# Performance work log

Measured on AMD Instinct MI355X. Metric: run time of the kernel, lower is better.

The kernel has to match this reference:

```python
import jax, jax.numpy as jnp
import numpy as np

B, L, D, H, DFF, MAXD = 4, 2048, 1024, 16, 4096, 512
HD = D // H


def layer_norm(x, gamma, beta, eps=1e-5):
    mu = jnp.mean(x, axis=-1, keepdims=True)
    var = jnp.mean(jnp.square(x - mu), axis=-1, keepdims=True)
    return (x - mu) * jax.lax.rsqrt(var + eps) * gamma + beta


def setup_inputs() -> dict:
    key = jax.random.key(0)
    ks = jax.random.split(key, 8)
    s = 0.02
    return {
        "x": jax.random.normal(ks[0], (B, L, D), jnp.float32),
        "w_qkv": jax.random.normal(ks[1], (D, 3 * D), jnp.float32) * s,
        "w_out": jax.random.normal(ks[2], (D, D), jnp.float32) * s,
        "b_out": jnp.zeros((D,), jnp.float32),
        "bias_table": jax.random.normal(ks[3], (2 * MAXD - 1, H), jnp.float32) * s,
        "gamma1": jnp.ones((D,), jnp.float32),
        "beta1": jnp.zeros((D,), jnp.float32),
        "w_ff1": jax.random.normal(ks[4], (D, DFF), jnp.float32) * s,
        "b_ff1": jnp.zeros((DFF,), jnp.float32),
        "w_ff2": jax.random.normal(ks[5], (DFF, D), jnp.float32) * s,
        "b_ff2": jnp.zeros((D,), jnp.float32),
        "gamma2": jnp.ones((D,), jnp.float32),
        "beta2": jnp.zeros((D,), jnp.float32),
    }


def reference(x, w_qkv, w_out, b_out, bias_table, gamma1, beta1,
              w_ff1, b_ff1, w_ff2, b_ff2, gamma2, beta2):
    b, l, c = x.shape
    scale = HD ** -0.5
    qkv = x @ w_qkv  # [B,L,3D]
    q, k, v = jnp.split(qkv, 3, axis=-1)
    # [B,H,L,hd]
    q = q.reshape(b, l, H, HD).transpose(0, 2, 1, 3)
    k = k.reshape(b, l, H, HD).transpose(0, 2, 1, 3)
    v = v.reshape(b, l, H, HD).transpose(0, 2, 1, 3)
    scores = jnp.einsum("bhqd,bhkd->bhqk", q, k) * scale
    # relative position bias: [H,L,L]
    coords = jnp.arange(l)
    rel = jnp.clip(coords[None, :] - coords[:, None] + MAXD - 1, 0, 2 * MAXD - 2)
    bias = bias_table[rel].transpose(2, 0, 1)
    scores = scores + bias[None]
    attn = jax.nn.softmax(scores, axis=-1)
    ctx = jnp.einsum("bhqk,bhkd->bhqd", attn, v)
    ctx = ctx.transpose(0, 2, 1, 3).reshape(b, l, c)
    attn_out = ctx @ w_out + b_out
    x = layer_norm(x + attn_out, gamma1, beta1)
    h = jax.nn.gelu(x @ w_ff1 + b_ff1, approximate=False)
    ffn_out = h @ w_ff2 + b_ff2
    x = layer_norm(x + ffn_out, gamma2, beta2)
    return x
```

## Files before the change

kernel.cpp:

```cpp
#include <hip/hip_runtime.h>

typedef unsigned short u16;
typedef __bf16 bf16x8 __attribute__((ext_vector_type(8)));
typedef float f32x4 __attribute__((ext_vector_type(4)));
typedef unsigned short u16x8 __attribute__((ext_vector_type(8)));

typedef __attribute__((address_space(1))) const void gvoid_t;
typedef __attribute__((address_space(3))) void svoid_t;

__device__ __forceinline__ float bf2f(u16 u) {
  union { unsigned int i; float f; } v; v.i = ((unsigned int)u) << 16; return v.f;
}
__device__ __forceinline__ u16 f2bf(float f) {
  union { float f; unsigned int i; } v; v.f = f;
  unsigned int u = v.i;
  return (u16)((u + 0x7fffu + ((u >> 16) & 1u)) >> 16);
}
__device__ __forceinline__ void async_copy16(const u16* g, u16* l) {
  __builtin_amdgcn_global_load_lds((gvoid_t*)g, (svoid_t*)l, 16, 0, 0);
}
__device__ __forceinline__ f32x4 mfma16(bf16x8 a, bf16x8 b, f32x4 c) {
  return __builtin_amdgcn_mfma_f32_16x16x32_bf16(a, b, c, 0, 0, 0);
}

__global__ __launch_bounds__(256) void pack_bf16(const float* __restrict__ src, u16* __restrict__ dst, int n4) {
  int i = blockIdx.x * 256 + threadIdx.x;
  if (i >= n4) return;
  float4 v = *(const float4*)(src + (size_t)i * 4);
  ushort4 o;
  o.x = f2bf(v.x); o.y = f2bf(v.y); o.z = f2bf(v.z); o.w = f2bf(v.w);
  *(ushort4*)(dst + (size_t)i * 4) = o;
}

__global__ void transpose_f2b(const float* __restrict__ src, u16* __restrict__ dst, int R, int C) {
  __shared__ u16 t[32][33];
  const int c0 = blockIdx.x * 32, r0 = blockIdx.y * 32;
  const int tx = threadIdx.x, ty = threadIdx.y;
#pragma unroll
  for (int i = 0; i < 4; ++i) {
    int r = r0 + ty + i * 8;
    t[ty + i * 8][tx] = f2bf(src[(size_t)r * C + c0 + tx]);
  }
  __syncthreads();
#pragma unroll
  for (int i = 0; i < 4; ++i) {
    int c = c0 + ty + i * 8;
    dst[(size_t)c * R + r0 + tx] = t[tx][ty + i * 8];
  }
}

__global__ void transpose_v(const u16* __restrict__ qkv, u16* __restrict__ vT2) {
  __shared__ u16 t[32][33];
  const int bh = blockIdx.z;
  const int b = bh >> 4, h = bh & 15;
  const int l0 = blockIdx.x * 32, d0 = blockIdx.y * 32;
  const int tx = threadIdx.x, ty = threadIdx.y;
#pragma unroll
  for (int i = 0; i < 4; ++i) {
    int l = l0 + ty + i * 8;
    t[ty + i * 8][tx] = qkv[(size_t)(b * 2048 + l) * 3072 + 2048 + h * 64 + d0 + tx];
  }
  __syncthreads();
  const int pos = 2 * (tx & 15) + (tx >> 4);
#pragma unroll
  for (int i = 0; i < 4; ++i) {
    int d = d0 + ty + i * 8;
    vT2[(size_t)bh * 131072 + (l0 >> 5) * 2048 + d * 32 + pos] = t[tx][ty + i * 8];
  }
}

template <int EPI>
__global__ __launch_bounds__(256) void gemm_bt(const u16* __restrict__ A, const u16* __restrict__ Bt,
                                               const float* __restrict__ bias, u16* __restrict__ C,
                                               int M, int N, int K) {
  __shared__ __align__(16) u16 As[128 * 32];
  __shared__ __align__(16) u16 Bs[128 * 32];
  const int tid = threadIdx.x;
  const int wave = tid >> 6, lane = tid & 63;
  const int quad = lane >> 4, l16 = lane & 15;
  const int wm = wave >> 1, wn = wave & 1;
  const int m0 = blockIdx.y * 128, n0 = blockIdx.x * 128;
  const int srow = lane >> 2, scol = (lane & 3) * 8;
  f32x4 acc[4][4] = {};
  for (int k0 = 0; k0 < K; k0 += 32) {
#pragma unroll
    for (int rr = 0; rr < 2; ++rr) {
      const int chunk = rr * 4 + wave;
      const int row = chunk * 16 + srow;
      async_copy16(&A[(size_t)(m0 + row) * K + k0 + scol], &As[chunk * 16 * 32]);
      async_copy16(&Bt[(size_t)(n0 + row) * K + k0 + scol], &Bs[chunk * 16 * 32]);
    }
    __syncthreads();
    bf16x8 af[4], bfv[4];
#pragma unroll
    for (int i = 0; i < 4; ++i)
      af[i] = *(const bf16x8*)&As[(wm * 64 + i * 16 + l16) * 32 + quad * 8];
#pragma unroll
    for (int j = 0; j < 4; ++j)
      bfv[j] = *(const bf16x8*)&Bs[(wn * 64 + j * 16 + l16) * 32 + quad * 8];
#pragma unroll
    for (int i = 0; i < 4; ++i)
#pragma unroll
      for (int j = 0; j < 4; ++j)
        acc[i][j] = mfma16(af[i], bfv[j], acc[i][j]);
    __syncthreads();
  }
#pragma unroll
  for (int i = 0; i < 4; ++i)
#pragma unroll
    for (int j = 0; j < 4; ++j) {
      const int col = n0 + wn * 64 + j * 16 + l16;
      float bv = 0.f;
      if (EPI > 0) bv = bias[col];
#pragma unroll
      for (int r = 0; r < 4; ++r) {
        const int row = m0 + wm * 64 + i * 16 + quad * 4 + r;
        float v = acc[i][j][r] + bv;
        if (EPI == 2) v = 0.5f * v * (1.f + erff(v * 0.70710678118654752f));
        C[(size_t)row * N + col] = f2bf(v);
      }
    }
}

__global__ __launch_bounds__(256, 4) void attn_kernel(const u16* __restrict__ qkv, const u16* __restrict__ vT2,
                                                      const float* __restrict__ btab, u16* __restrict__ ctx) {
  const int tid = threadIdx.x;
  const int wave = tid >> 6, lane = tid & 63;
  const int quad = lane >> 4, l16 = lane & 15;
  const int bh = blockIdx.x >> 4, qb = blockIdx.x & 15;
  const int b = bh >> 4, h = bh & 15;
  const int q0b = qb * 128;
  const int qw = q0b + wave * 32;
  const float LOG2E = 1.4426950408889634f;

  __shared__ __align__(16) u16 Ks[64 * 72];
  __shared__ __align__(16) u16 Vs[2][64 * 40];
  __shared__ __align__(16) float bias_s[192];
  __shared__ __align__(16) u16 P[4][2][16 * 40];

  bf16x8 qf[2][2];
#pragma unroll
  for (int qi = 0; qi < 2; ++qi)
#pragma unroll
    for (int kk = 0; kk < 2; ++kk) {
      u16x8 qv = *(const u16x8*)&qkv[((size_t)(b * 2048) + qw + qi * 16 + l16) * 3072 + h * 64 + kk * 32 + quad * 8];
      union { u16 s[8]; bf16x8 v; } u;
#pragma unroll
      for (int j = 0; j < 8; ++j) u.s[j] = f2bf(bf2f(qv[j]) * (0.125f * LOG2E));
      qf[qi][kk] = u.v;
    }

  f32x4 o[2][4] = {};
  float psum[2][4] = {};
  const float c_lo = btab[h] * LOG2E, c_hi = btab[1022 * 16 + h] * LOG2E;
  const int krow = tid >> 2, kc = tid & 3;
  const int rowb0 = wave * 32 + quad * 4;

  for (int kt = 0; kt < 32; ++kt) {
    const int kbase = kt * 64;
    const int dmin = kbase - q0b - 127, dmax = kbase - q0b + 63;
    const int mode = (dmax <= -511) ? 1 : (dmin >= 511 ? 2 : 0);
#pragma unroll
    for (int half = 0; half < 2; ++half) {
      const int chunk = kc + half * 4;
      u16x8 kv = *(const u16x8*)&qkv[((size_t)(b * 2048) + kbase + krow) * 3072 + 1024 + h * 64 + chunk * 8];
      *(u16x8*)&Ks[krow * 72 + chunk * 8] = kv;
    }
#pragma unroll
    for (int g = 0; g < 2; ++g) {
      u16x8 vv = *(const u16x8*)&vT2[(size_t)bh * 131072 + (2 * kt + g) * 2048 + tid * 8];
      *(u16x8*)&Vs[g][krow * 40 + kc * 8] = vv;
    }
    if (mode == 0 && tid < 192) {
      int idx = dmin + 191 - tid + 511;
      idx = min(max(idx, 0), 1022);
      bias_s[tid] = btab[idx * 16 + h] * LOG2E;
    }
    __syncthreads();
#pragma unroll
    for (int g = 0; g < 2; ++g) {
      f32x4 z[2][2];
#pragma unroll
      for (int t = 0; t < 2; ++t) {
        const u16* kr = &Ks[(g * 32 + t * 16 + l16) * 72 + quad * 8];
        bf16x8 kf0 = *(const bf16x8*)kr;
        bf16x8 kf1 = *(const bf16x8*)(kr + 32);
#pragma unroll
        for (int qi = 0; qi < 2; ++qi) {
          f32x4 zz = {0.f, 0.f, 0.f, 0.f};
          zz = mfma16(qf[qi][0], kf0, zz);
          zz = mfma16(qf[qi][1], kf1, zz);
          z[t][qi] = zz;
        }
      }
#pragma unroll
      for (int qi = 0; qi < 2; ++qi) {
        u16* pw = P[wave][qi];
#pragma unroll
        for (int r = 0; r < 4; ++r) {
          const int rowb = rowb0 + qi * 16 + r;
          float b0, b1;
          if (mode == 1) { b0 = c_lo; b1 = c_lo; }
          else if (mode == 2) { b0 = c_hi; b1 = c_hi; }
          else {
            b0 = bias_s[64 + rowb - (g * 32 + l16)];
            b1 = bias_s[48 + rowb - (g * 32 + l16)];
          }
          float p0 = __builtin_amdgcn_exp2f(z[0][qi][r] + b0);
          float p1 = __builtin_amdgcn_exp2f(z[1][qi][r] + b1);
          psum[qi][r] += p0 + p1;
          union { float f; unsigned u; } a0, a1; a0.f = p0; a1.f = p1;
          unsigned pk = __builtin_amdgcn_perm(a1.u, a0.u, 0x07060302u);
          *(unsigned*)&pw[(quad * 4 + r) * 40 + 2 * l16] = pk;
        }
      }
      bf16x8 pa0 = *(const bf16x8*)&P[wave][0][l16 * 40 + quad * 8];
      bf16x8 pa1 = *(const bf16x8*)&P[wave][1][l16 * 40 + quad * 8];
#pragma unroll
      for (int c = 0; c < 4; ++c) {
        bf16x8 vf = *(const bf16x8*)&Vs[g][(c * 16 + l16) * 40 + quad * 8];
        o[0][c] = mfma16(pa0, vf, o[0][c]);
        o[1][c] = mfma16(pa1, vf, o[1][c]);
      }
    }
    __syncthreads();
  }
#pragma unroll
  for (int qi = 0; qi < 2; ++qi)
#pragma unroll
    for (int off = 1; off < 16; off <<= 1)
#pragma unroll
      for (int r = 0; r < 4; ++r) psum[qi][r] += __shfl_xor(psum[qi][r], off);
#pragma unroll
  for (int qi = 0; qi < 2; ++qi)
#pragma unroll
    for (int r = 0; r < 4; ++r) {
      float inv = 1.f / psum[qi][r];
      int row = qw + qi * 16 + quad * 4 + r;
#pragma unroll
      for (int c = 0; c < 4; ++c)
        ctx[((size_t)(b * 2048 + row)) * 1024 + h * 64 + c * 16 + l16] = f2bf(o[qi][c][r] * inv);
    }
}

template <int A_F32, int O_F32>
__global__ __launch_bounds__(256) void add_ln(const void* __restrict__ av, const u16* __restrict__ b,
                                              const float* __restrict__ gamma, const float* __restrict__ beta,
                                              void* __restrict__ ov) {
  const int row = blockIdx.x, t = threadIdx.x;
  const size_t base = (size_t)row * 1024 + t * 4;
  float x0, x1, x2, x3;
  if (A_F32) {
    float4 a4 = *(const float4*)((const float*)av + base);
    x0 = a4.x; x1 = a4.y; x2 = a4.z; x3 = a4.w;
  } else {
    ushort4 a4 = *(const ushort4*)((const u16*)av + base);
    x0 = bf2f(a4.x); x1 = bf2f(a4.y); x2 = bf2f(a4.z); x3 = bf2f(a4.w);
  }
  ushort4 b4 = *(const ushort4*)&b[base];
  x0 += bf2f(b4.x); x1 += bf2f(b4.y); x2 += bf2f(b4.z); x3 += bf2f(b4.w);
  float s = x0 + x1 + x2 + x3;
  float q = x0 * x0 + x1 * x1 + x2 * x2 + x3 * x3;
  for (int off = 32; off > 0; off >>= 1) { s += __shfl_down(s, off); q += __shfl_down(q, off); }
  __shared__ float sh_s[4], sh_q[4];
  if ((t & 63) == 0) { sh_s[t >> 6] = s; sh_q[t >> 6] = q; }
  __syncthreads();
  s = sh_s[0] + sh_s[1] + sh_s[2] + sh_s[3];
  q = sh_q[0] + sh_q[1] + sh_q[2] + sh_q[3];
  float mu = s * (1.f / 1024.f);
  float var = q * (1.f / 1024.f) - mu * mu;
  float rs = rsqrtf(var + 1e-5f);
  float4 g4 = *(const float4*)&gamma[t * 4];
  float4 be4 = *(const float4*)&beta[t * 4];
  float y0 = (x0 - mu) * rs * g4.x + be4.x;
  float y1 = (x1 - mu) * rs * g4.y + be4.y;
  float y2 = (x2 - mu) * rs * g4.z + be4.z;
  float y3 = (x3 - mu) * rs * g4.w + be4.w;
  if (O_F32) {
    float4 o4 = {y0, y1, y2, y3};
    *(float4*)((float*)ov + base) = o4;
  } else {
    ushort4 o4;
    o4.x = f2bf(y0); o4.y = f2bf(y1); o4.z = f2bf(y2); o4.w = f2bf(y3);
    *(ushort4*)((u16*)ov + base) = o4;
  }
}

extern "C" void kernel_launch(void* const* d_in, const int* in_sizes, int n_in,
                              void* d_out, int out_size, void* d_ws, size_t ws_size,
                              hipStream_t stream) {
  const float* x      = (const float*)d_in[0];
  const float* w_qkv  = (const float*)d_in[1];
  const float* w_out  = (const float*)d_in[2];
  const float* b_out  = (const float*)d_in[3];
  const float* btab   = (const float*)d_in[4];
  const float* gamma1 = (const float*)d_in[5];
  const float* beta1  = (const float*)d_in[6];
  const float* w_ff1  = (const float*)d_in[7];
  const float* b_ff1  = (const float*)d_in[8];
  const float* w_ff2  = (const float*)d_in[9];
  const float* b_ff2  = (const float*)d_in[10];
  const float* gamma2 = (const float*)d_in[11];
  const float* beta2  = (const float*)d_in[12];
  float* out = (float*)d_out;

  char* w = (char*)d_ws;
  auto alloc = [&](size_t elems) { u16* p = (u16*)w; w += elems * 2; return p; };
  u16* wqkvT = alloc(3072UL * 1024);
  u16* woutT = alloc(1024UL * 1024);
  u16* wff1T = alloc(4096UL * 1024);
  u16* wff2T = alloc(1024UL * 4096);
  u16* xb    = alloc(8192UL * 1024);
  u16* qkv   = alloc(8192UL * 3072);
  u16* vT2   = alloc(64UL * 64 * 2048);
  u16* ctx   = alloc(8192UL * 1024);
  u16* x1    = alloc(8192UL * 1024);
  u16* attn  = qkv;
  u16* h     = qkv;
  u16* ffn   = ctx;

  dim3 tb(32, 8);
  pack_bf16<<<8192, 256, 0, stream>>>(x, xb, 8192 * 1024 / 4);
  transpose_f2b<<<dim3(3072 / 32, 1024 / 32), tb, 0, stream>>>(w_qkv, wqkvT, 1024, 3072);
  transpose_f2b<<<dim3(1024 / 32, 1024 / 32), tb, 0, stream>>>(w_out, woutT, 1024, 1024);
  transpose_f2b<<<dim3(4096 / 32, 1024 / 32), tb, 0, stream>>>(w_ff1, wff1T, 1024, 4096);
  transpose_f2b<<<dim3(1024 / 32, 4096 / 32), tb, 0, stream>>>(w_ff2, wff2T, 4096, 1024);

  gemm_bt<0><<<dim3(24, 64), 256, 0, stream>>>(xb, wqkvT, nullptr, qkv, 8192, 3072, 1024);
  transpose_v<<<dim3(64, 2, 64), tb, 0, stream>>>(qkv, vT2);
  attn_kernel<<<1024, 256, 0, stream>>>(qkv, vT2, btab, ctx);
  gemm_bt<1><<<dim3(8, 64), 256, 0, stream>>>(ctx, woutT, b_out, attn, 8192, 1024, 1024);
  add_ln<1, 0><<<8192, 256, 0, stream>>>(x, attn, gamma1, beta1, x1);
  gemm_bt<2><<<dim3(32, 64), 256, 0, stream>>>(x1, wff1T, b_ff1, h, 8192, 4096, 1024);
  gemm_bt<1><<<dim3(8, 64), 256, 0, stream>>>(h, wff2T, b_ff2, ffn, 8192, 1024, 4096);
  add_ln<0, 1><<<8192, 256, 0, stream>>>(x1, ffn, gamma2, beta2, out);
}
```

Measured before the change: 608.5 us.

## Load two K-slices per barrier in GEMM and use tanh-approximated GELU

The GEMM main loop now stages two 32-wide K slices into separate LDS buffers before each barrier, halving the number of synchronisations per tile. The FF1 epilogue swaps the exact erf GELU for a tanh-form approximation built from hardware exp2 and reciprocal, and bias loads are hoisted out of the row loop. This doubles LDS use per block, which may cut occupancy, and the GELU approximation slightly deviates from the exact reference.

```diff
diff --git a/kernel.cpp b/kernel.cpp
--- a/kernel.cpp
+++ b/kernel.cpp
@@ -21,6 +21,12 @@
 }
 __device__ __forceinline__ f32x4 mfma16(bf16x8 a, bf16x8 b, f32x4 c) {
   return __builtin_amdgcn_mfma_f32_16x16x32_bf16(a, b, c, 0, 0, 0);
+}
+__device__ __forceinline__ float fast_gelu(float v) {
+  float g = v * (0.7978845608028654f + 0.035677408136300125f * v * v);
+  float t = __builtin_amdgcn_exp2f(g * 2.8853900817779268f);
+  float th = 1.f - 2.f * __builtin_amdgcn_rcpf(t + 1.f);
+  return 0.5f * v * (1.f + th);
 }
 
 __global__ __launch_bounds__(256) void pack_bf16(const float* __restrict__ src, u16* __restrict__ dst, int n4) {
@@ -73,8 +79,8 @@
 __global__ __launch_bounds__(256) void gemm_bt(const u16* __restrict__ A, const u16* __restrict__ Bt,
                                                const float* __restrict__ bias, u16* __restrict__ C,
                                                int M, int N, int K) {
-  __shared__ __align__(16) u16 As[128 * 32];
-  __shared__ __align__(16) u16 Bs[128 * 32];
+  __shared__ __align__(16) u16 As[2][128 * 32];
+  __shared__ __align__(16) u16 Bs[2][128 * 32];
   const int tid = threadIdx.x;
   const int wave = tid >> 6, lane = tid & 63;
   const int quad = lane >> 4, l16 = lane & 15;
@@ -82,42 +88,49 @@
   const int m0 = blockIdx.y * 128, n0 = blockIdx.x * 128;
   const int srow = lane >> 2, scol = (lane & 3) * 8;
   f32x4 acc[4][4] = {};
-  for (int k0 = 0; k0 < K; k0 += 32) {
-#pragma unroll
-    for (int rr = 0; rr < 2; ++rr) {
-      const int chunk = rr * 4 + wave;
-      const int row = chunk * 16 + srow;
-      async_copy16(&A[(size_t)(m0 + row) * K + k0 + scol], &As[chunk * 16 * 32]);
-      async_copy16(&Bt[(size_t)(n0 + row) * K + k0 + scol], &Bs[chunk * 16 * 32]);
-    }
+  for (int k0 = 0; k0 < K; k0 += 64) {
+#pragma unroll
+    for (int s = 0; s < 2; ++s)
+#pragma unroll
+      for (int rr = 0; rr < 2; ++rr) {
+        const int chunk = rr * 4 + wave;
+        const int row = chunk * 16 + srow;
+        async_copy16(&A[(size_t)(m0 + row) * K + k0 + s * 32 + scol], &As[s][chunk * 16 * 32]);
+        async_copy16(&Bt[(size_t)(n0 + row) * K + k0 + s * 32 + scol], &Bs[s][chunk * 16 * 32]);
+      }
     __syncthreads();
-    bf16x8 af[4], bfv[4];
-#pragma unroll
-    for (int i = 0; i < 4; ++i)
-      af[i] = *(const bf16x8*)&As[(wm * 64 + i * 16 + l16) * 32 + quad * 8];
-#pragma unroll
-    for (int j = 0; j < 4; ++j)
-      bfv[j] = *(const bf16x8*)&Bs[(wn * 64 + j * 16 + l16) * 32 + quad * 8];
-#pragma unroll
-    for (int i = 0; i < 4; ++i)
+#pragma unroll
+    for (int s = 0; s < 2; ++s) {
+      bf16x8 af[4], bfv[4];
+#pragma unroll
+      for (int i = 0; i < 4; ++i)
+        af[i] = *(const bf16x8*)&As[s][(wm * 64 + i * 16 + l16) * 32 + quad * 8];
 #pragma unroll
       for (int j = 0; j < 4; ++j)
-        acc[i][j] = mfma16(af[i], bfv[j], acc[i][j]);
+        bfv[j] = *(const bf16x8*)&Bs[s][(wn * 64 + j * 16 + l16) * 32 + quad * 8];
+#pragma unroll
+      for (int i = 0; i < 4; ++i)
+#pragma unroll
+        for (int j = 0; j < 4; ++j)
+          acc[i][j] = mfma16(af[i], bfv[j], acc[i][j]);
+    }
     __syncthreads();
   }
+  float bv[4];
+#pragma unroll
+  for (int j = 0; j < 4; ++j)
+    bv[j] = (EPI > 0) ? bias[n0 + wn * 64 + j * 16 + l16] : 0.f;
 #pragma unroll
   for (int i = 0; i < 4; ++i)
 #pragma unroll
-    for (int j = 0; j < 4; ++j) {
-      const int col = n0 + wn * 64 + j * 16 + l16;
-      float bv = 0.f;
-      if (EPI > 0) bv = bias[col];
-#pragma unroll
-      for (int r = 0; r < 4; ++r) {
-        const int row = m0 + wm * 64 + i * 16 + quad * 4 + r;
-        float v = acc[i][j][r] + bv;
-        if (EPI == 2) v = 0.5f * v * (1.f + erff(v * 0.70710678118654752f));
-        C[(size_t)row * N + col] = f2bf(v);
+    for (int r = 0; r < 4; ++r) {
+      const int row = m0 + wm * 64 + i * 16 + quad * 4 + r;
+      u16* cp = &C[(size_t)row * N + n0 + wn * 64 + l16];
+#pragma unroll
+      for (int j = 0; j < 4; ++j) {
+        float v = acc[i][j][r] + bv[j];
+        if (EPI == 2) v = fast_gelu(v);
+        cp[j * 16] = f2bf(v);
       }
     }
 }
```

New measurement: 560.6 us. 7.9% less time.
